# Kernel tuning notes

Measured on AMD Instinct MI355X. Metric: run time of the kernel, lower is better.

The kernel has to match this reference:

```python
import jax, jax.numpy as jnp
import numpy as np


def setup_inputs() -> dict:
    key = jax.random.key(0)
    k1, k2 = jax.random.split(key)
    N, C, H, W = 4, 64, 128, 256
    x = jax.random.normal(k1, (N, C, H, W), dtype=jnp.float32)
    y = jax.random.normal(k2, (N, C, H, W), dtype=jnp.float32)
    return {"x": x, "y": y, "maxdisp": 48}


def reference(x, y, maxdisp):
    # corr[n, i, h, w] = sum_c x[n,c,h,w] * y[n,c,h,w-i]  (zero where w-i < 0)
    # Matches the torch loop: y is left-padded by maxdisp-1 zeros, and output
    # channel i (loop d = maxdisp-1-i, reversed) takes slice d : d+W of y_pad.
    D = int(maxdisp)
    N, C, H, W = x.shape
    y_pad = jnp.pad(y, ((0, 0), (0, 0), (0, 0), (D - 1, 0)))  # [N,C,H,W+D-1]
    corr_slices = []
    for i in range(D):  # fixed small disparity set, not a data dim
        y_slice = jax.lax.slice_in_dim(y_pad, D - 1 - i, D - 1 - i + W, axis=3)
        corr_slices.append(jnp.einsum('nchw,nchw->nhw', x, y_slice))
    corr = jnp.stack(corr_slices, axis=1)  # [N,D,H,W]
    return corr
```

## Files before the change

### kernel.cpp

```cpp
#include <hip/hip_runtime.h>

#define N_ 4
#define C_ 64
#define H_ 128
#define W_ 256
#define D_ 48
#define HW_ (H_ * W_)

#define WTILE 128
#define HALO  D_
#define YCOLS (WTILE + HALO)
#define CCHUNK 16
#define NCHUNK (C_ / CCHUNK)
#define VT 4
#define DT 12
#define NIG (D_ / DT)
#define NTW (WTILE / VT)
#define NTHREADS (NTW * NIG)

__global__ __launch_bounds__(NTHREADS, 2)
void corr1d_v2(const float* __restrict__ x,
               const float* __restrict__ y,
               float* __restrict__ out) {
    __shared__ __align__(16) float ysh[CCHUNK][YCOLS];
    __shared__ __align__(16) float xsh[CCHUNK][WTILE];

    const int t  = threadIdx.x;
    const int tw = t & (NTW - 1);
    const int ig = t >> 5;
    const int b  = blockIdx.x;
    const int wt = (b & 1) * WTILE;
    const int nh = b >> 1;
    const int n  = nh / H_;
    const int h  = nh % H_;

    const size_t in_base = ((size_t)n * C_ * H_ + h) * W_;

    const int i0 = ig * DT;
    const int w0 = wt + tw * VT;

    float acc[DT][VT];
    #pragma unroll
    for (int k = 0; k < DT; ++k)
        #pragma unroll
        for (int v = 0; v < VT; ++v) acc[k][v] = 0.f;

    const int js = 4 * tw - DT * ig + (HALO - DT + 1) - 1;

    for (int ch = 0; ch < NCHUNK; ++ch) {
        const int c0 = ch * CCHUNK;

        #pragma unroll
        for (int kk = 0; kk < 6; ++kk) {
            int idx = kk * NTHREADS + t;
            if (idx < CCHUNK * (YCOLS / 4)) {
                int r = idx / (YCOLS / 4);
                int q = idx % (YCOLS / 4);
                int w = wt - HALO + 4 * q;
                float4 v;
                if (w >= 0)
                    v = *reinterpret_cast<const float4*>(
                        &y[in_base + (size_t)(c0 + r) * HW_ + w]);
                else
                    v = make_float4(0.f, 0.f, 0.f, 0.f);
                *reinterpret_cast<float4*>(&ysh[r][4 * q]) = v;
            }
        }
        #pragma unroll
        for (int kk = 0; kk < 4; ++kk) {
            int idx = kk * NTHREADS + t;
            int r = idx / (WTILE / 4);
            int q = idx % (WTILE / 4);
            float4 v = *reinterpret_cast<const float4*>(
                &x[in_base + (size_t)(c0 + r) * HW_ + wt + 4 * q]);
            *reinterpret_cast<float4*>(&xsh[r][4 * q]) = v;
        }
        __syncthreads();

        #pragma unroll 4
        for (int cc = 0; cc < CCHUNK; ++cc) {
            const float4 q0 = *reinterpret_cast<const float4*>(&ysh[cc][js]);
            const float4 q1 = *reinterpret_cast<const float4*>(&ysh[cc][js + 4]);
            const float4 q2 = *reinterpret_cast<const float4*>(&ysh[cc][js + 8]);
            const float4 q3 = *reinterpret_cast<const float4*>(&ysh[cc][js + 12]);
            const float4 xq = *reinterpret_cast<const float4*>(&xsh[cc][tw * VT]);
            const float r_[16] = {q0.x, q0.y, q0.z, q0.w,
                                  q1.x, q1.y, q1.z, q1.w,
                                  q2.x, q2.y, q2.z, q2.w,
                                  q3.x, q3.y, q3.z, q3.w};
            const float xv[VT] = {xq.x, xq.y, xq.z, xq.w};
            #pragma unroll
            for (int k = 0; k < DT; ++k)
                #pragma unroll
                for (int v = 0; v < VT; ++v)
                    acc[k][v] = fmaf(xv[v], r_[12 + v - k], acc[k][v]);
        }
        __syncthreads();
    }

    const size_t ob = ((size_t)(n * D_ + i0) * H_ + h) * W_ + w0;
    #pragma unroll
    for (int k = 0; k < DT; ++k) {
        float4 o;
        o.x = acc[k][0]; o.y = acc[k][1]; o.z = acc[k][2]; o.w = acc[k][3];
        *reinterpret_cast<float4*>(&out[ob + (size_t)k * HW_]) = o;
    }
}

extern "C" void kernel_launch(void* const* d_in, const int* in_sizes, int n_in,
                              void* d_out, int out_size, void* d_ws, size_t ws_size,
                              hipStream_t stream) {
    (void)in_sizes; (void)n_in; (void)out_size; (void)d_ws; (void)ws_size;
    const float* x = (const float*)d_in[0];
    const float* y = (const float*)d_in[1];
    float* out = (float*)d_out;

    dim3 grid(N_ * H_ * (W_ / WTILE));
    dim3 block(NTHREADS);
    corr1d_v2<<<grid, block, 0, stream>>>(x, y, out);
}
```

Before: 117.7 us.

## Double-buffer y tile in LDS with register prefetch; read x directly per channel

The y halo tile moves to a double-buffered shared-memory layout. The next channel chunk is loaded into registers while the current chunk is computed, and one barrier per chunk replaces two. The x tile no longer goes through shared memory: each thread loads its own float4 of x straight from global memory, one channel ahead. This is meant to hide global load latency and cut LDS traffic and barriers, at the cost of extra registers for the prefetch (which may hurt occupancy) and many small per-channel global loads of x.

```diff
diff --git a/kernel.cpp b/kernel.cpp
--- a/kernel.cpp
+++ b/kernel.cpp
@@ -14,16 +14,17 @@
 #define NCHUNK (C_ / CCHUNK)
 #define VT 4
 #define DT 12
+#define NTW (WTILE / VT)
 #define NIG (D_ / DT)
-#define NTW (WTILE / VT)
 #define NTHREADS (NTW * NIG)
+#define YF4 (CCHUNK * (YCOLS / 4))
+#define NPREF ((YF4 + NTHREADS - 1) / NTHREADS)
 
 __global__ __launch_bounds__(NTHREADS, 2)
-void corr1d_v2(const float* __restrict__ x,
+void corr1d_v3(const float* __restrict__ x,
                const float* __restrict__ y,
                float* __restrict__ out) {
-    __shared__ __align__(16) float ysh[CCHUNK][YCOLS];
-    __shared__ __align__(16) float xsh[CCHUNK][WTILE];
+    __shared__ __align__(16) float ysh[2][CCHUNK][YCOLS];
 
     const int t  = threadIdx.x;
     const int tw = t & (NTW - 1);
@@ -35,9 +36,9 @@
     const int h  = nh % H_;
 
     const size_t in_base = ((size_t)n * C_ * H_ + h) * W_;
-
     const int i0 = ig * DT;
     const int w0 = wt + tw * VT;
+    const int js = 4 * tw - DT * ig + (HALO - DT);
 
     float acc[DT][VT];
     #pragma unroll
@@ -45,45 +46,66 @@
         #pragma unroll
         for (int v = 0; v < VT; ++v) acc[k][v] = 0.f;
 
-    const int js = 4 * tw - DT * ig + (HALO - DT + 1) - 1;
+    float4 yp[NPREF];
+
+    #pragma unroll
+    for (int kk = 0; kk < NPREF; ++kk) {
+        int idx = kk * NTHREADS + t;
+        if (idx < YF4) {
+            int r = idx / (YCOLS / 4);
+            int q = idx % (YCOLS / 4);
+            int w = wt - HALO + 4 * q;
+            yp[kk] = (w >= 0)
+                ? *reinterpret_cast<const float4*>(&y[in_base + (size_t)r * HW_ + w])
+                : make_float4(0.f, 0.f, 0.f, 0.f);
+        }
+    }
+    #pragma unroll
+    for (int kk = 0; kk < NPREF; ++kk) {
+        int idx = kk * NTHREADS + t;
+        if (idx < YF4) {
+            int r = idx / (YCOLS / 4);
+            int q = idx % (YCOLS / 4);
+            *reinterpret_cast<float4*>(&ysh[0][r][4 * q]) = yp[kk];
+        }
+    }
+    __syncthreads();
+
+    float4 xn = *reinterpret_cast<const float4*>(&x[in_base + w0]);
 
     for (int ch = 0; ch < NCHUNK; ++ch) {
-        const int c0 = ch * CCHUNK;
+        const int cur = ch & 1;
+
+        if (ch + 1 < NCHUNK) {
+            const int c0n = (ch + 1) * CCHUNK;
+            #pragma unroll
+            for (int kk = 0; kk < NPREF; ++kk) {
+                int idx = kk * NTHREADS + t;
+                if (idx < YF4) {
+                    int r = idx / (YCOLS / 4);
+                    int q = idx % (YCOLS / 4);
+                    int w = wt - HALO + 4 * q;
+                    yp[kk] = (w >= 0)
+                        ? *reinterpret_cast<const float4*>(
+                              &y[in_base + (size_t)(c0n + r) * HW_ + w])
+                        : make_float4(0.f, 0.f, 0.f, 0.f);
+                }
+            }
+        }
 
         #pragma unroll
-        for (int kk = 0; kk < 6; ++kk) {
-            int idx = kk * NTHREADS + t;
-            if (idx < CCHUNK * (YCOLS / 4)) {
-                int r = idx / (YCOLS / 4);
-                int q = idx % (YCOLS / 4);
-                int w = wt - HALO + 4 * q;
-                float4 v;
-                if (w >= 0)
-                    v = *reinterpret_cast<const float4*>(
-                        &y[in_base + (size_t)(c0 + r) * HW_ + w]);
-                else
-                    v = make_float4(0.f, 0.f, 0.f, 0.f);
-                *reinterpret_cast<float4*>(&ysh[r][4 * q]) = v;
-            }
-        }
-        #pragma unroll
-        for (int kk = 0; kk < 4; ++kk) {
-            int idx = kk * NTHREADS + t;
-            int r = idx / (WTILE / 4);
-            int q = idx % (WTILE / 4);
-            float4 v = *reinterpret_cast<const float4*>(
-                &x[in_base + (size_t)(c0 + r) * HW_ + wt + 4 * q]);
-            *reinterpret_cast<float4*>(&xsh[r][4 * q]) = v;
-        }
-        __syncthreads();
+        for (int cc = 0; cc < CCHUNK; ++cc) {
+            const float4 xq = xn;
+            const int c = ch * CCHUNK + cc;
+            if (c + 1 < C_)
+                xn = *reinterpret_cast<const float4*>(
+                    &x[in_base + (size_t)(c + 1) * HW_ + w0]);
 
-        #pragma unroll 4
-        for (int cc = 0; cc < CCHUNK; ++cc) {
-            const float4 q0 = *reinterpret_cast<const float4*>(&ysh[cc][js]);
-            const float4 q1 = *reinterpret_cast<const float4*>(&ysh[cc][js + 4]);
-            const float4 q2 = *reinterpret_cast<const float4*>(&ysh[cc][js + 8]);
-            const float4 q3 = *reinterpret_cast<const float4*>(&ysh[cc][js + 12]);
-            const float4 xq = *reinterpret_cast<const float4*>(&xsh[cc][tw * VT]);
+            const float* yr = &ysh[cur][cc][js];
+            const float4 q0 = *reinterpret_cast<const float4*>(yr);
+            const float4 q1 = *reinterpret_cast<const float4*>(yr + 4);
+            const float4 q2 = *reinterpret_cast<const float4*>(yr + 8);
+            const float4 q3 = *reinterpret_cast<const float4*>(yr + 12);
             const float r_[16] = {q0.x, q0.y, q0.z, q0.w,
                                   q1.x, q1.y, q1.z, q1.w,
                                   q2.x, q2.y, q2.z, q2.w,
@@ -95,7 +117,19 @@
                 for (int v = 0; v < VT; ++v)
                     acc[k][v] = fmaf(xv[v], r_[12 + v - k], acc[k][v]);
         }
-        __syncthreads();
+
+        if (ch + 1 < NCHUNK) {
+            #pragma unroll
+            for (int kk = 0; kk < NPREF; ++kk) {
+                int idx = kk * NTHREADS + t;
+                if (idx < YF4) {
+                    int r = idx / (YCOLS / 4);
+                    int q = idx % (YCOLS / 4);
+                    *reinterpret_cast<float4*>(&ysh[cur ^ 1][r][4 * q]) = yp[kk];
+                }
+            }
+            __syncthreads();
+        }
     }
 
     const size_t ob = ((size_t)(n * D_ + i0) * H_ + h) * W_ + w0;
@@ -117,5 +151,5 @@
 
     dim3 grid(N_ * H_ * (W_ / WTILE));
     dim3 block(NTHREADS);
-    corr1d_v2<<<grid, block, 0, stream>>>(x, y, out);
+    corr1d_v3<<<grid, block, 0, stream>>>(x, y, out);
 }
```

After: 276.7 us. 135% more time.

## Double-buffer LDS staging with direct global-to-LDS loads and full-row blocks

Applied to the files above, without the earlier changes.

Each block now covers a whole image row (256 threads, one wave per disparity group). The y and x chunks are staged straight into LDS with global_load_lds, and two buffers let the next channel chunk load while the current one is computed. Instead of a zero-filled halo, out-of-range y columns are clamped and the invalid outputs are masked to zero at store time. This aims to remove the register round-trip and the stall on every load, and to drop the redundant halo loads. In exchange it doubles LDS use and halves the block count, which may lower occupancy.

```diff
diff --git a/kernel.cpp b/kernel.cpp
--- a/kernel.cpp
+++ b/kernel.cpp
@@ -7,37 +7,57 @@
 #define D_ 48
 #define HW_ (H_ * W_)
 
-#define WTILE 128
-#define HALO  D_
-#define YCOLS (WTILE + HALO)
+#define YCOLS 320
 #define CCHUNK 16
 #define NCHUNK (C_ / CCHUNK)
 #define VT 4
 #define DT 12
+#define NTW (W_ / VT)
 #define NIG (D_ / DT)
-#define NTW (WTILE / VT)
 #define NTHREADS (NTW * NIG)
+#define YSPW 5
+#define XSPW 4
+
+typedef __attribute__((address_space(3))) void* as3p;
+typedef const __attribute__((address_space(1))) void* as1p;
+
+__device__ __forceinline__ void gl_lds16(const float* g, const float* l) {
+    __builtin_amdgcn_global_load_lds((as1p)(const void*)g, (as3p)(void*)l, 16, 0, 0);
+}
 
 __global__ __launch_bounds__(NTHREADS, 2)
-void corr1d_v2(const float* __restrict__ x,
+void corr1d_v4(const float* __restrict__ x,
                const float* __restrict__ y,
                float* __restrict__ out) {
-    __shared__ __align__(16) float ysh[CCHUNK][YCOLS];
-    __shared__ __align__(16) float xsh[CCHUNK][WTILE];
+    __shared__ __align__(16) float ysh[2][CCHUNK][YCOLS];
+    __shared__ __align__(16) float xsh[2][CCHUNK][W_];
 
-    const int t  = threadIdx.x;
-    const int tw = t & (NTW - 1);
-    const int ig = t >> 5;
-    const int b  = blockIdx.x;
-    const int wt = (b & 1) * WTILE;
-    const int nh = b >> 1;
-    const int n  = nh / H_;
-    const int h  = nh % H_;
-
+    const int t    = threadIdx.x;
+    const int lane = t & 63;
+    const int wv   = t >> 6;
+    const int tw   = lane;
+    const int ig   = wv;
+    const int nh   = blockIdx.x;
+    const int n    = nh / H_;
+    const int h    = nh % H_;
     const size_t in_base = ((size_t)n * C_ * H_ + h) * W_;
 
-    const int i0 = ig * DT;
-    const int w0 = wt + tw * VT;
+    int yrow[YSPW], ywoff[YSPW];
+    #pragma unroll
+    for (int s = 0; s < YSPW; ++s) {
+        int idx = (wv * YSPW + s) * 64 + lane;
+        int r = idx / 80;
+        int q = idx - r * 80;
+        int w = 4 * q - D_;
+        if (w < 0) w = 0;
+        if (w > W_ - 4) w = W_ - 4;
+        yrow[s] = r;
+        ywoff[s] = w;
+    }
+
+    float* yflat = &ysh[0][0][0];
+
+    const int js = 4 * tw - DT * ig + (D_ - DT);
 
     float acc[DT][VT];
     #pragma unroll
@@ -45,45 +65,38 @@
         #pragma unroll
         for (int v = 0; v < VT; ++v) acc[k][v] = 0.f;
 
-    const int js = 4 * tw - DT * ig + (HALO - DT + 1) - 1;
+    auto stage = [&](int buf, int c0) {
+        #pragma unroll
+        for (int s = 0; s < YSPW; ++s) {
+            const float* g = y + in_base + (size_t)(c0 + yrow[s]) * HW_ + ywoff[s];
+            const float* l = yflat + (size_t)buf * (CCHUNK * YCOLS)
+                                   + (wv * YSPW + s) * 256;
+            gl_lds16(g, l);
+        }
+        #pragma unroll
+        for (int s = 0; s < XSPW; ++s) {
+            int r = wv * XSPW + s;
+            const float* g = x + in_base + (size_t)(c0 + r) * HW_ + 4 * lane;
+            const float* l = &xsh[buf][r][0];
+            gl_lds16(g, l);
+        }
+    };
+
+    stage(0, 0);
+    __syncthreads();
 
     for (int ch = 0; ch < NCHUNK; ++ch) {
-        const int c0 = ch * CCHUNK;
+        const int cur = ch & 1;
+        if (ch + 1 < NCHUNK) stage(cur ^ 1, (ch + 1) * CCHUNK);
 
         #pragma unroll
-        for (int kk = 0; kk < 6; ++kk) {
-            int idx = kk * NTHREADS + t;
-            if (idx < CCHUNK * (YCOLS / 4)) {
-                int r = idx / (YCOLS / 4);
-                int q = idx % (YCOLS / 4);
-                int w = wt - HALO + 4 * q;
-                float4 v;
-                if (w >= 0)
-                    v = *reinterpret_cast<const float4*>(
-                        &y[in_base + (size_t)(c0 + r) * HW_ + w]);
-                else
-                    v = make_float4(0.f, 0.f, 0.f, 0.f);
-                *reinterpret_cast<float4*>(&ysh[r][4 * q]) = v;
-            }
-        }
-        #pragma unroll
-        for (int kk = 0; kk < 4; ++kk) {
-            int idx = kk * NTHREADS + t;
-            int r = idx / (WTILE / 4);
-            int q = idx % (WTILE / 4);
-            float4 v = *reinterpret_cast<const float4*>(
-                &x[in_base + (size_t)(c0 + r) * HW_ + wt + 4 * q]);
-            *reinterpret_cast<float4*>(&xsh[r][4 * q]) = v;
-        }
-        __syncthreads();
-
-        #pragma unroll 4
         for (int cc = 0; cc < CCHUNK; ++cc) {
-            const float4 q0 = *reinterpret_cast<const float4*>(&ysh[cc][js]);
-            const float4 q1 = *reinterpret_cast<const float4*>(&ysh[cc][js + 4]);
-            const float4 q2 = *reinterpret_cast<const float4*>(&ysh[cc][js + 8]);
-            const float4 q3 = *reinterpret_cast<const float4*>(&ysh[cc][js + 12]);
-            const float4 xq = *reinterpret_cast<const float4*>(&xsh[cc][tw * VT]);
+            const float* yr = &ysh[cur][cc][js];
+            const float4 q0 = *reinterpret_cast<const float4*>(yr);
+            const float4 q1 = *reinterpret_cast<const float4*>(yr + 4);
+            const float4 q2 = *reinterpret_cast<const float4*>(yr + 8);
+            const float4 q3 = *reinterpret_cast<const float4*>(yr + 12);
+            const float4 xq = *reinterpret_cast<const float4*>(&xsh[cur][cc][4 * tw]);
             const float r_[16] = {q0.x, q0.y, q0.z, q0.w,
                                   q1.x, q1.y, q1.z, q1.w,
                                   q2.x, q2.y, q2.z, q2.w,
@@ -95,14 +108,18 @@
                 for (int v = 0; v < VT; ++v)
                     acc[k][v] = fmaf(xv[v], r_[12 + v - k], acc[k][v]);
         }
-        __syncthreads();
+        if (ch + 1 < NCHUNK) __syncthreads();
     }
 
-    const size_t ob = ((size_t)(n * D_ + i0) * H_ + h) * W_ + w0;
+    const size_t ob = ((size_t)(n * D_ + ig * DT) * H_ + h) * W_ + 4 * tw;
     #pragma unroll
     for (int k = 0; k < DT; ++k) {
+        const int ik = ig * DT + k;
         float4 o;
-        o.x = acc[k][0]; o.y = acc[k][1]; o.z = acc[k][2]; o.w = acc[k][3];
+        o.x = (4 * tw + 0 >= ik) ? acc[k][0] : 0.f;
+        o.y = (4 * tw + 1 >= ik) ? acc[k][1] : 0.f;
+        o.z = (4 * tw + 2 >= ik) ? acc[k][2] : 0.f;
+        o.w = (4 * tw + 3 >= ik) ? acc[k][3] : 0.f;
         *reinterpret_cast<float4*>(&out[ob + (size_t)k * HW_]) = o;
     }
 }
@@ -115,7 +132,7 @@
     const float* y = (const float*)d_in[1];
     float* out = (float*)d_out;
 
-    dim3 grid(N_ * H_ * (W_ / WTILE));
+    dim3 grid(N_ * H_);
     dim3 block(NTHREADS);
-    corr1d_v2<<<grid, block, 0, stream>>>(x, y, out);
+    corr1d_v4<<<grid, block, 0, stream>>>(x, y, out);
 }
```

Result: slower. 197.3 us (+67.6%).
